# Performance work log

Measured on AMD Instinct MI355X. Metric: run time of the kernel, lower is better.

Reference implementation:

```python
import jax, jax.numpy as jnp
import numpy as np
import math

B, S, D, H = 2, 2048, 2048, 16
DH = D // H
NEG = -1e9  # finite stand-in for -inf so fully-masked rows stay NaN-free


def setup_inputs() -> dict:
    key = jax.random.key(0)
    ks = jax.random.split(key, 6)
    x = jax.random.normal(ks[0], (B, S, D), dtype=jnp.float32)
    key_padding_mask = jax.random.randint(ks[1], (B, S), 0, 2, dtype=jnp.int32)
    Wqkv_w = jax.random.normal(ks[2], (3 * D, D), dtype=jnp.float32) / math.sqrt(D)
    Wqkv_b = jnp.zeros((3 * D,), dtype=jnp.float32)
    out_w = jax.random.normal(ks[3], (D, D), dtype=jnp.float32) / math.sqrt(D)
    out_b = jnp.zeros((D,), dtype=jnp.float32)
    return {"x": x, "key_padding_mask": key_padding_mask, "Wqkv_w": Wqkv_w,
            "Wqkv_b": Wqkv_b, "out_w": out_w, "out_b": out_b}


def reference(x, key_padding_mask, Wqkv_w, Wqkv_b, out_w, out_b):
    b, s, d = x.shape
    # fused QKV projection (torch Linear: y = x @ W.T + b)
    qkv = (x @ Wqkv_w.T + Wqkv_b).reshape(b, s, 3, H, DH)
    q, k, v = qkv[:, :, 0], qkv[:, :, 1], qkv[:, :, 2]  # each [b, s, H, DH]
    scale = 1.0 / math.sqrt(DH)
    scores = jnp.einsum('bqhd,bkhd->bhqk', q, k) * scale  # [b, H, s, s]
    # additive key-padding bias: -inf where mask == 0 (finite NEG for stability)
    pad_bias = jnp.where(key_padding_mask == 0, NEG, 0.0).astype(x.dtype)[:, None, None, :]
    # causal mask: key index > query index is disallowed
    causal = jnp.where(jnp.arange(s)[None, :] > jnp.arange(s)[:, None], NEG, 0.0).astype(x.dtype)
    p = jax.nn.softmax(scores + pad_bias + causal, axis=-1)
    attn = jnp.einsum('bhqk,bkhd->bqhd', p, v).reshape(b, s, d)
    return attn @ out_w.T + out_b
```

## Files before the change

### kernel.cpp

```cpp
#include <hip/hip_runtime.h>
#include <cstdint>

typedef unsigned short u16;
typedef __attribute__((ext_vector_type(8))) short short8v;
typedef __attribute__((ext_vector_type(8))) unsigned short u16x8;
typedef __attribute__((ext_vector_type(4))) float floatx4;

typedef unsigned int __attribute__((address_space(1))) as1_u32;
typedef unsigned int __attribute__((address_space(3))) as3_u32;

__device__ __forceinline__ u16 f2bf(float f) {
  union { float f; unsigned u; } v; v.f = f;
  unsigned r = v.u + 0x7FFFu + ((v.u >> 16) & 1u);
  return (u16)(r >> 16);
}

__device__ __forceinline__ unsigned cvt_pk_bf16(float lo, float hi) {
  unsigned r;
  asm("v_cvt_pk_bf16_f32 %0, %1, %2" : "=v"(r) : "v"(lo), "v"(hi));
  return r;
}

__device__ __forceinline__ void gload16(void* lds, const void* g) {
  __builtin_amdgcn_global_load_lds((as1_u32*)(uintptr_t)g, (as3_u32*)(uintptr_t)lds, 16, 0, 0);
}

__global__ __launch_bounds__(256) void f2bf_kernel(const float* __restrict__ in,
                                                   u16* __restrict__ out, int n4) {
  int i = blockIdx.x * 256 + threadIdx.x;
  const int stride = gridDim.x * 256;
  for (; i < n4; i += stride) {
    float4 v = ((const float4*)in)[i];
    ushort4 o;
    o.x = f2bf(v.x); o.y = f2bf(v.y); o.z = f2bf(v.z); o.w = f2bf(v.w);
    ((ushort4*)out)[i] = o;
  }
}

template <int OUT_BF16>
__global__ __launch_bounds__(256)
void gemm_bt(const u16* __restrict__ A, const u16* __restrict__ B,
             const float* __restrict__ bias, void* __restrict__ C,
             int M, int N, int K) {
  __shared__ u16 As[128 * 32];
  __shared__ u16 Bs[128 * 32];
  const int tid = threadIdx.x;
  const int wave = tid >> 6, lane = tid & 63;
  const int wr = wave >> 1, wc = wave & 1;
  const int li = lane & 15, lg = lane >> 4;
  const int brow = blockIdx.y * 128, bcol = blockIdx.x * 128;

  const int e0 = tid * 8, e1 = 2048 + tid * 8;
  const u16* aSrc0 = A + (size_t)(brow + (e0 >> 5)) * K + (e0 & 31);
  const u16* aSrc1 = A + (size_t)(brow + (e1 >> 5)) * K + (e1 & 31);
  const u16* bSrc0 = B + (size_t)(bcol + (e0 >> 5)) * K + (e0 & 31);
  const u16* bSrc1 = B + (size_t)(bcol + (e1 >> 5)) * K + (e1 & 31);

  floatx4 acc[4][4];
#pragma unroll
  for (int m = 0; m < 4; ++m)
#pragma unroll
    for (int n = 0; n < 4; ++n) acc[m][n] = floatx4{0.f, 0.f, 0.f, 0.f};

  for (int kt = 0; kt < K; kt += 32) {
    gload16((char*)As + tid * 16,        aSrc0 + kt);
    gload16((char*)As + 4096 + tid * 16, aSrc1 + kt);
    gload16((char*)Bs + tid * 16,        bSrc0 + kt);
    gload16((char*)Bs + 4096 + tid * 16, bSrc1 + kt);
    asm volatile("s_waitcnt vmcnt(0)" ::: "memory");
    __syncthreads();

    short8v a[4], b[4];
#pragma unroll
    for (int m = 0; m < 4; ++m)
      a[m] = *(const short8v*)&As[(wr * 64 + m * 16 + li) * 32 + lg * 8];
#pragma unroll
    for (int n = 0; n < 4; ++n)
      b[n] = *(const short8v*)&Bs[(wc * 64 + n * 16 + li) * 32 + lg * 8];
#pragma unroll
    for (int m = 0; m < 4; ++m)
#pragma unroll
      for (int n = 0; n < 4; ++n)
        acc[m][n] = __builtin_amdgcn_mfma_f32_16x16x32_bf16(a[m], b[n], acc[m][n], 0, 0, 0);
    __syncthreads();
  }

  const int crow0 = brow + wr * 64 + lg * 4;
  const int ccol0 = bcol + wc * 64 + li;
#pragma unroll
  for (int n = 0; n < 4; ++n) {
    const float bv = bias[ccol0 + n * 16];
#pragma unroll
    for (int m = 0; m < 4; ++m) {
#pragma unroll
      for (int j = 0; j < 4; ++j) {
        const float v = acc[m][n][j] + bv;
        const size_t idx = (size_t)(crow0 + m * 16 + j) * N + (ccol0 + n * 16);
        if (OUT_BF16) ((u16*)C)[idx] = f2bf(v);
        else          ((float*)C)[idx] = v;
      }
    }
  }
}

__global__ __launch_bounds__(256)
void transpose_v(const u16* __restrict__ qkv, u16* __restrict__ vt) {
  __shared__ u16 T[64][136];
  const int st = blockIdx.x, bh = blockIdx.y;
  const int b = bh >> 4, h = bh & 15;
  const int tid = threadIdx.x;
  const u16* src = qkv + (size_t)(b * 2048 + st * 64) * 6144 + 4096 + h * 128;
  u16* dst = vt + (size_t)bh * 128 * 2048 + st * 64;
#pragma unroll
  for (int p = 0; p < 4; ++p) {
    const int e = (p * 256 + tid) * 8;
    const int r = e >> 7, c = e & 127;
    *(u16x8*)&T[r][c] = *(const u16x8*)&src[(size_t)r * 6144 + c];
  }
  __syncthreads();
#pragma unroll
  for (int p = 0; p < 4; ++p) {
    const int e = (p * 256 + tid) * 8;
    const int dh = e >> 6, s0 = e & 63;
    u16x8 o;
#pragma unroll
    for (int j = 0; j < 8; ++j) o[j] = T[s0 + j][dh];
    *(u16x8*)&dst[(size_t)dh * 2048 + s0] = o;
  }
}

__global__ __launch_bounds__(256, 2)
void attn_fused(const u16* __restrict__ qkv, const u16* __restrict__ vt,
                const int* __restrict__ kpm, u16* __restrict__ attn_out) {
  constexpr int S = 2048, DQ = 6144;
  __shared__ u16 Kl[2][64 * 128];
  __shared__ u16 Vl[128 * 64];
  __shared__ float mskf[2048];
  __shared__ int s_any;
  const int bx = blockIdx.x, by = blockIdx.y;
  const int qt = ((by >> 4) & 1) ? bx : (15 - bx);
  const int bh = by;
  const int b = bh >> 4, h = bh & 15;
  const int tid = threadIdx.x, wave = tid >> 6, lane = tid & 63;
  const int lg = lane >> 4, li = lane & 15;
  const int qrow0 = qt * 128 + wave * 32;

  const u16* Qb = qkv + (size_t)b * S * DQ + h * 128;
  const u16* Kb = Qb + 2048;
  const u16* Vtb = vt + (size_t)bh * 128 * 2048;
  const int* mrow = kpm + b * S;

  if (tid == 0) s_any = 0;
  __syncthreads();
  {
    int a = 0;
    for (int j = tid; j < 2048; j += 256) {
      const int mv = mrow[j];
      mskf[j] = mv ? 0.f : -1.0e9f;
      if (mv && j <= qt * 128) a = 1;
    }
    if (a) s_any = 1;
  }
  __syncthreads();
  const int anyv = s_any;
  const int nt = anyv ? (2 * qt + 2) : 32;
  const int causalFromW = anyv ? (qrow0 >> 6) : 0;

  short8v qb[2][4];
#pragma unroll
  for (int m = 0; m < 2; ++m) {
    const u16* qp = Qb + (size_t)(qrow0 + m * 16 + li) * DQ + lg * 8;
#pragma unroll
    for (int kk = 0; kk < 4; ++kk) qb[m][kk] = *(const short8v*)(qp + kk * 32);
  }
  asm volatile("s_waitcnt vmcnt(0)" ::: "memory");

  float mM[2], lSum[2];
  floatx4 oa[2][8];
#pragma unroll
  for (int m = 0; m < 2; ++m) {
    mM[m] = -3.0e38f; lSum[m] = 0.f;
#pragma unroll
    for (int n = 0; n < 8; ++n) oa[m][n] = floatx4{0.f, 0.f, 0.f, 0.f};
  }

  const u16* kSrc[4]; const u16* vSrc[4];
#pragma unroll
  for (int i = 0; i < 4; ++i) {
    const int L = i * 4096 + tid * 16;
    const int r = L >> 8;
    const int c = ((L & 255) ^ ((r & 7) << 4)) >> 1;
    kSrc[i] = Kb + (size_t)r * DQ + c;
    const int d = L >> 7;
    const int sv = ((L & 127) ^ ((d & 7) << 4)) >> 1;
    vSrc[i] = Vtb + (size_t)d * 2048 + sv;
  }

#define STAGE_K(buf, kt_)                                                      \
  {                                                                            \
    const int kv0_ = (kt_) * 64;                                               \
    _Pragma("unroll")                                                          \
    for (int i = 0; i < 4; ++i)                                                \
      gload16((char*)Kl + (buf) * 16384 + i * 4096 + tid * 16,                 \
              kSrc[i] + (size_t)kv0_ * DQ);                                    \
  }
#define STAGE_V(kt_)                                                           \
  {                                                                            \
    const int kv0_ = (kt_) * 64;                                               \
    _Pragma("unroll")                                                          \
    for (int i = 0; i < 4; ++i)                                                \
      gload16((char*)Vl + i * 4096 + tid * 16, vSrc[i] + kv0_);                \
  }

  const float scale = 0.08838834764831845f;

  STAGE_K(0, 0);
  STAGE_V(0);

  for (int kt = 0; kt < nt; ++kt) {
    const int cur = kt & 1;
    const int kv0 = kt * 64;
    if (kt + 1 < nt) {
      STAGE_K(cur ^ 1, kt + 1);
      asm volatile("s_waitcnt vmcnt(8)" ::: "memory");
    } else {
      asm volatile("s_waitcnt vmcnt(4)" ::: "memory");
    }
    __builtin_amdgcn_s_barrier();

    const char* Kcur = (const char*)Kl + cur * 16384;

    floatx4 sc[2][4];
#pragma unroll
    for (int n = 0; n < 4; ++n) { sc[0][n] = floatx4{0,0,0,0}; sc[1][n] = floatx4{0,0,0,0}; }
#pragma unroll
    for (int n = 0; n < 4; ++n) {
      const int r = n * 16 + li;
#pragma unroll
      for (int kk = 0; kk < 4; ++kk) {
        const int byteo = (r * 256 + kk * 64 + lg * 16) ^ ((r & 7) << 4);
        const short8v kf = *(const short8v*)(Kcur + byteo);
        sc[0][n] = __builtin_amdgcn_mfma_f32_16x16x32_bf16(kf, qb[0][kk], sc[0][n], 0, 0, 0);
        sc[1][n] = __builtin_amdgcn_mfma_f32_16x16x32_bf16(kf, qb[1][kk], sc[1][n], 0, 0, 0);
      }
    }

    floatx4 pbv[4];
#pragma unroll
    for (int n = 0; n < 4; ++n)
      pbv[n] = *(const floatx4*)&mskf[kv0 + n * 16 + lg * 4];
    const bool cz = (kt >= causalFromW);

    short8v pf[2][2];
#pragma unroll
    for (int m = 0; m < 2; ++m) {
      const int q_l = qrow0 + m * 16 + li;
      float tmax = -3.0e38f;
#pragma unroll
      for (int n = 0; n < 4; ++n)
#pragma unroll
        for (int j = 0; j < 4; ++j) {
          float s = sc[m][n][j] * scale + pbv[n][j];
          if (cz && (kv0 + n * 16 + lg * 4 + j > q_l)) s -= 1.0e9f;
          sc[m][n][j] = s;
          tmax = fmaxf(tmax, s);
        }
      tmax = fmaxf(tmax, __shfl_xor(tmax, 16));
      tmax = fmaxf(tmax, __shfl_xor(tmax, 32));
      const float mnew = fmaxf(mM[m], tmax);
      const float f = __expf(mM[m] - mnew);
      mM[m] = mnew;
      float rs = 0.f;
#pragma unroll
      for (int n = 0; n < 4; ++n)
#pragma unroll
        for (int j = 0; j < 4; ++j) {
          const float e = __expf(sc[m][n][j] - mnew);
          sc[m][n][j] = e; rs += e;
        }
      rs += __shfl_xor(rs, 16);
      rs += __shfl_xor(rs, 32);
      lSum[m] = lSum[m] * f + rs;
#pragma unroll
      for (int n2 = 0; n2 < 8; ++n2) oa[m][n2] *= f;

      unsigned w32[4][2];
#pragma unroll
      for (int n = 0; n < 4; ++n) {
        w32[n][0] = cvt_pk_bf16(sc[m][n][0], sc[m][n][1]);
        w32[n][1] = cvt_pk_bf16(sc[m][n][2], sc[m][n][3]);
      }
      union PF { short8v s; unsigned w[4]; } pfu[2];
#pragma unroll
      for (int kk2 = 0; kk2 < 2; ++kk2) {
#pragma unroll
        for (int hh = 0; hh < 2; ++hh) {
          unsigned u = w32[2 * kk2][hh], v = w32[2 * kk2 + 1][hh];
          asm volatile("v_permlane32_swap_b32 %0, %1" : "+v"(u), "+v"(v));
          asm volatile("v_permlane16_swap_b32 %0, %1" : "+v"(u), "+v"(v));
          pfu[kk2].w[hh] = u;
          pfu[kk2].w[2 + hh] = v;
        }
      }
      pf[m][0] = pfu[0].s;
      pf[m][1] = pfu[1].s;
    }

    if (kt + 1 < nt) asm volatile("s_waitcnt vmcnt(4)" ::: "memory");
    else             asm volatile("s_waitcnt vmcnt(0)" ::: "memory");
    __builtin_amdgcn_s_barrier();

#pragma unroll
    for (int kk2 = 0; kk2 < 2; ++kk2) {
#pragma unroll
      for (int n2 = 0; n2 < 8; ++n2) {
        const int d = n2 * 16 + li;
        const int vbyte = (d * 128 + kk2 * 64 + lg * 16) ^ ((d & 7) << 4);
        const short8v vf = *(const short8v*)((const char*)Vl + vbyte);
        oa[0][n2] = __builtin_amdgcn_mfma_f32_16x16x32_bf16(vf, pf[0][kk2], oa[0][n2], 0, 0, 0);
        oa[1][n2] = __builtin_amdgcn_mfma_f32_16x16x32_bf16(vf, pf[1][kk2], oa[1][n2], 0, 0, 0);
      }
    }
    __builtin_amdgcn_s_barrier();
    if (kt + 1 < nt) STAGE_V(kt + 1);
  }

  {
    char* Ol = (char*)Kl + wave * 8192;
#pragma unroll
    for (int m = 0; m < 2; ++m) {
      const float inv = 1.0f / lSum[m];
      const int q_ = m * 16 + li;
#pragma unroll
      for (int n2 = 0; n2 < 8; ++n2) {
        unsigned lo = cvt_pk_bf16(oa[m][n2][0] * inv, oa[m][n2][1] * inv);
        unsigned hi = cvt_pk_bf16(oa[m][n2][2] * inv, oa[m][n2][3] * inv);
        const int byteo = (q_ * 256 + n2 * 32 + lg * 8) ^ ((q_ & 7) << 4);
        uint2 pr; pr.x = lo; pr.y = hi;
        *(uint2*)(Ol + byteo) = pr;
      }
    }
    asm volatile("s_waitcnt lgkmcnt(0)" ::: "memory");
#pragma unroll
    for (int rr = 0; rr < 4; ++rr) {
      const int r = rr * 8 + (lane >> 3);
      const size_t grow = (size_t)(b * 2048 + qt * 128 + wave * 32 + r) * 2048 + h * 128;
#pragma unroll
      for (int s2 = 0; s2 < 2; ++s2) {
        const int byteo = (r * 256 + (lane & 7) * 32 + s2 * 16) ^ ((r & 7) << 4);
        const u16x8 val = *(const u16x8*)(Ol + byteo);
        *(u16x8*)&attn_out[grow + (lane & 7) * 16 + s2 * 8] = val;
      }
    }
  }
#undef STAGE_K
#undef STAGE_V
}

extern "C" void kernel_launch(void* const* d_in, const int* in_sizes, int n_in,
                              void* d_out, int out_size, void* d_ws, size_t ws_size,
                              hipStream_t stream) {
  const float* x    = (const float*)d_in[0];
  const int*   kpm  = (const int*)d_in[1];
  const float* wqkv = (const float*)d_in[2];
  const float* bqkv = (const float*)d_in[3];
  const float* wout = (const float*)d_in[4];
  const float* bout = (const float*)d_in[5];
  float* out = (float*)d_out;

  char* ws = (char*)d_ws;
  u16* xbf   = (u16*)(ws);
  u16* wqbf  = (u16*)(ws + (16u << 20));
  u16* wobf  = (u16*)(ws + (40u << 20));
  u16* qkvb  = (u16*)(ws + (48u << 20));
  u16* vtb   = (u16*)(ws + (96u << 20));
  u16* attnb = (u16*)(ws + (112u << 20));

  f2bf_kernel<<<1024, 256, 0, stream>>>(x,    xbf,  4096 * 2048 / 4);
  f2bf_kernel<<<1024, 256, 0, stream>>>(wqkv, wqbf, 6144 * 2048 / 4);
  f2bf_kernel<<<1024, 256, 0, stream>>>(wout, wobf, 2048 * 2048 / 4);

  gemm_bt<1><<<dim3(48, 32), 256, 0, stream>>>(xbf, wqbf, bqkv, qkvb, 4096, 6144, 2048);
  transpose_v<<<dim3(32, 32), 256, 0, stream>>>(qkvb, vtb);
  attn_fused<<<dim3(16, 32), 256, 0, stream>>>(qkvb, vtb, kpm, attnb);
  gemm_bt<0><<<dim3(16, 32), 256, 0, stream>>>(attnb, wobf, bout, out, 4096, 2048, 2048);
}
```

Measured before the change: 341.7 us.

## Replace GEMM with 256x256-tile, 8-wave, double-buffered swizzled LDS pipeline

Replaces the 128x128 single-buffered GEMM with a 256x256 tile kernel using 512 threads. It uses a 64-wide K step, XOR-swizzled LDS, and double-buffered global-to-LDS loads staggered across four compute phases, with setprio around the MFMA bursts. The aim is to hide global load latency, raise arithmetic intensity and cut bank conflicts. The larger tiles leave only 128 blocks for the output projection, which may underfill the device, and the kernel uses heavy LDS and registers.

```diff
diff --git a/kernel.cpp b/kernel.cpp
--- a/kernel.cpp
+++ b/kernel.cpp
@@ -38,60 +38,120 @@
 }
 
 template <int OUT_BF16>
-__global__ __launch_bounds__(256)
-void gemm_bt(const u16* __restrict__ A, const u16* __restrict__ B,
+__global__ __launch_bounds__(512, 2)
+void gemm256(const u16* __restrict__ A, const u16* __restrict__ B,
              const float* __restrict__ bias, void* __restrict__ C,
              int M, int N, int K) {
-  __shared__ u16 As[128 * 32];
-  __shared__ u16 Bs[128 * 32];
+  __shared__ u16 lds[2][4][8192];
   const int tid = threadIdx.x;
-  const int wave = tid >> 6, lane = tid & 63;
-  const int wr = wave >> 1, wc = wave & 1;
+  const int wid = tid >> 6, lane = tid & 63;
+  const int wr = wid >> 2, wc = wid & 3;
   const int li = lane & 15, lg = lane >> 4;
-  const int brow = blockIdx.y * 128, bcol = blockIdx.x * 128;
-
-  const int e0 = tid * 8, e1 = 2048 + tid * 8;
-  const u16* aSrc0 = A + (size_t)(brow + (e0 >> 5)) * K + (e0 & 31);
-  const u16* aSrc1 = A + (size_t)(brow + (e1 >> 5)) * K + (e1 & 31);
-  const u16* bSrc0 = B + (size_t)(bcol + (e0 >> 5)) * K + (e0 & 31);
-  const u16* bSrc1 = B + (size_t)(bcol + (e1 >> 5)) * K + (e1 & 31);
-
-  floatx4 acc[4][4];
-#pragma unroll
-  for (int m = 0; m < 4; ++m)
+  const int brow = blockIdx.y * 256, bcol = blockIdx.x * 256;
+  const int NT = K >> 6;
+
+  const int rowL = tid >> 3;
+  const int klog = ((((tid & 7) << 4) ^ ((rowL & 7) << 4)) >> 1);
+  const u16* aS = A + (size_t)(brow + rowL) * K + klog;
+  const u16* bS = B + (size_t)(bcol + rowL) * K + klog;
+
+#define STG(slot, reg, src, hh, kt_)                                            \
+  {                                                                             \
+    const u16* s_ = (src) + (size_t)((hh) * 128) * K + (kt_) * 64;              \
+    gload16((char*)&lds[slot][reg][0] + tid * 16, s_);                          \
+    gload16((char*)&lds[slot][reg][0] + 8192 + tid * 16, s_ + (size_t)64 * K);  \
+  }
+
+  floatx4 acc[8][4];
+#pragma unroll
+  for (int m = 0; m < 8; ++m)
 #pragma unroll
     for (int n = 0; n < 4; ++n) acc[m][n] = floatx4{0.f, 0.f, 0.f, 0.f};
 
-  for (int kt = 0; kt < K; kt += 32) {
-    gload16((char*)As + tid * 16,        aSrc0 + kt);
-    gload16((char*)As + 4096 + tid * 16, aSrc1 + kt);
-    gload16((char*)Bs + tid * 16,        bSrc0 + kt);
-    gload16((char*)Bs + 4096 + tid * 16, bSrc1 + kt);
-    asm volatile("s_waitcnt vmcnt(0)" ::: "memory");
-    __syncthreads();
-
-    short8v a[4], b[4];
-#pragma unroll
-    for (int m = 0; m < 4; ++m)
-      a[m] = *(const short8v*)&As[(wr * 64 + m * 16 + li) * 32 + lg * 8];
-#pragma unroll
-    for (int n = 0; n < 4; ++n)
-      b[n] = *(const short8v*)&Bs[(wc * 64 + n * 16 + li) * 32 + lg * 8];
-#pragma unroll
-    for (int m = 0; m < 4; ++m)
-#pragma unroll
-      for (int n = 0; n < 4; ++n)
-        acc[m][n] = __builtin_amdgcn_mfma_f32_16x16x32_bf16(a[m], b[n], acc[m][n], 0, 0, 0);
-    __syncthreads();
-  }
-
-  const int crow0 = brow + wr * 64 + lg * 4;
+  const int kx0 = (lg * 16) ^ ((li & 7) << 4);
+  const int kx1 = (64 + lg * 16) ^ ((li & 7) << 4);
+  const int ar0 = li * 128;
+  const int bc0 = ((wc & 1) * 64 + li) * 128;
+
+  STG(0, 0, aS, 0, 0);
+  STG(0, 1, aS, 1, 0);
+  STG(0, 2, bS, 0, 0);
+  STG(0, 3, bS, 1, 0);
+  STG(1, 2, bS, 0, 1);
+  STG(1, 3, bS, 1, 1);
+  asm volatile("s_waitcnt vmcnt(4)" ::: "memory");
+  __builtin_amdgcn_s_barrier();
+
+  for (int t = 0; t < NT; ++t) {
+    const int cur = t & 1;
+    const char* Ab = (const char*)&lds[cur][wr][0];
+    const char* Bb = (const char*)&lds[cur][2 + (wc >> 1)][0];
+
+    short8v bf[4][2], af[2][2];
+#pragma unroll
+    for (int n = 0; n < 4; ++n) {
+      bf[n][0] = *(const short8v*)(Bb + bc0 + n * 2048 + kx0);
+      bf[n][1] = *(const short8v*)(Bb + bc0 + n * 2048 + kx1);
+    }
+#pragma unroll
+    for (int mm = 0; mm < 2; ++mm) {
+      af[mm][0] = *(const short8v*)(Ab + ar0 + mm * 2048 + kx0);
+      af[mm][1] = *(const short8v*)(Ab + ar0 + mm * 2048 + kx1);
+    }
+    if (t + 1 < NT) STG(cur ^ 1, 0, aS, 0, t + 1);
+    asm volatile("s_waitcnt lgkmcnt(8)" ::: "memory");
+    __builtin_amdgcn_s_barrier();
+    asm volatile("s_waitcnt lgkmcnt(0)" ::: "memory");
+    __builtin_amdgcn_s_setprio(1);
+#pragma unroll
+    for (int mm = 0; mm < 2; ++mm)
+#pragma unroll
+      for (int ks = 0; ks < 2; ++ks)
+#pragma unroll
+        for (int n = 0; n < 4; ++n)
+          acc[mm][n] = __builtin_amdgcn_mfma_f32_16x16x32_bf16(af[mm][ks], bf[n][ks], acc[mm][n], 0, 0, 0);
+    __builtin_amdgcn_s_setprio(0);
+    __builtin_amdgcn_s_barrier();
+
+#pragma unroll
+    for (int ph = 1; ph < 4; ++ph) {
+      const int m0 = ph * 2;
+      short8v a2[2][2];
+#pragma unroll
+      for (int mm = 0; mm < 2; ++mm) {
+        a2[mm][0] = *(const short8v*)(Ab + ar0 + (m0 + mm) * 2048 + kx0);
+        a2[mm][1] = *(const short8v*)(Ab + ar0 + (m0 + mm) * 2048 + kx1);
+      }
+      if (ph == 1)      { if (t + 1 < NT) STG(cur ^ 1, 1, aS, 1, t + 1); }
+      else if (ph == 2) { if (t + 2 < NT) STG(cur, 2, bS, 0, t + 2); }
+      else              { if (t + 2 < NT) STG(cur, 3, bS, 1, t + 2); }
+      __builtin_amdgcn_s_barrier();
+      asm volatile("s_waitcnt lgkmcnt(0)" ::: "memory");
+      __builtin_amdgcn_s_setprio(1);
+#pragma unroll
+      for (int mm = 0; mm < 2; ++mm)
+#pragma unroll
+        for (int ks = 0; ks < 2; ++ks)
+#pragma unroll
+          for (int n = 0; n < 4; ++n)
+            acc[m0 + mm][n] = __builtin_amdgcn_mfma_f32_16x16x32_bf16(a2[mm][ks], bf[n][ks], acc[m0 + mm][n], 0, 0, 0);
+      __builtin_amdgcn_s_setprio(0);
+      if (ph == 3) {
+        if (t + 2 < NT) asm volatile("s_waitcnt vmcnt(4)" ::: "memory");
+        else            asm volatile("s_waitcnt vmcnt(0)" ::: "memory");
+      }
+      __builtin_amdgcn_s_barrier();
+    }
+  }
+#undef STG
+
+  const int crow0 = brow + wr * 128 + lg * 4;
   const int ccol0 = bcol + wc * 64 + li;
 #pragma unroll
   for (int n = 0; n < 4; ++n) {
     const float bv = bias[ccol0 + n * 16];
 #pragma unroll
-    for (int m = 0; m < 4; ++m) {
+    for (int m = 0; m < 8; ++m) {
 #pragma unroll
       for (int j = 0; j < 4; ++j) {
         const float v = acc[m][n][j] + bv;
@@ -380,8 +440,8 @@
   f2bf_kernel<<<1024, 256, 0, stream>>>(wqkv, wqbf, 6144 * 2048 / 4);
   f2bf_kernel<<<1024, 256, 0, stream>>>(wout, wobf, 2048 * 2048 / 4);
 
-  gemm_bt<1><<<dim3(48, 32), 256, 0, stream>>>(xbf, wqbf, bqkv, qkvb, 4096, 6144, 2048);
+  gemm256<1><<<dim3(24, 16), 512, 0, stream>>>(xbf, wqbf, bqkv, qkvb, 4096, 6144, 2048);
   transpose_v<<<dim3(32, 32), 256, 0, stream>>>(qkvb, vtb);
   attn_fused<<<dim3(16, 32), 256, 0, stream>>>(qkvb, vtb, kpm, attnb);
-  gemm_bt<0><<<dim3(16, 32), 256, 0, stream>>>(attnb, wobf, bout, out, 4096, 2048, 2048);
-}
+  gemm256<0><<<dim3(8, 16), 512, 0, stream>>>(attnb, wobf, bout, out, 4096, 2048, 2048);
+}
```

New measurement: 315.5 us. 1.08x faster.

## Replace GEMM with 256x256-tile, triple-buffered, swizzled-LDS 1024-thread kernel

Applied to the files above, without the earlier changes.

Replaces the 128x128 single-buffered GEMM used for both the QKV and output projections with a 256x256-tile kernel run by 16 waves. The kernel keeps three LDS stages, issuing global-to-LDS loads two K-steps ahead so memory latency overlaps the MFMA work, and it drops one of the two barriers per step. It also XOR-swizzles the LDS layout to avoid bank conflicts, remaps block IDs so neighbouring blocks share inputs in L2, and raises wave priority around the MFMA block. In exchange, the output GEMM now launches only 128 large blocks, which can leave many CUs idle, and the 96KB LDS footprint limits occupancy.

```diff
diff --git a/kernel.cpp b/kernel.cpp
--- a/kernel.cpp
+++ b/kernel.cpp
@@ -38,23 +38,36 @@
 }
 
 template <int OUT_BF16>
-__global__ __launch_bounds__(256)
-void gemm_bt(const u16* __restrict__ A, const u16* __restrict__ B,
+__global__ __launch_bounds__(1024, 4)
+void gemm_v3(const u16* __restrict__ A, const u16* __restrict__ B,
              const float* __restrict__ bias, void* __restrict__ C,
              int M, int N, int K) {
-  __shared__ u16 As[128 * 32];
-  __shared__ u16 Bs[128 * 32];
+  __shared__ u16 Al[3][8192];
+  __shared__ u16 Bl[3][8192];
   const int tid = threadIdx.x;
-  const int wave = tid >> 6, lane = tid & 63;
-  const int wr = wave >> 1, wc = wave & 1;
+  const int wid = tid >> 6, lane = tid & 63;
+  const int wr = wid >> 2, wc = wid & 3;
   const int li = lane & 15, lg = lane >> 4;
-  const int brow = blockIdx.y * 128, bcol = blockIdx.x * 128;
-
-  const int e0 = tid * 8, e1 = 2048 + tid * 8;
-  const u16* aSrc0 = A + (size_t)(brow + (e0 >> 5)) * K + (e0 & 31);
-  const u16* aSrc1 = A + (size_t)(brow + (e1 >> 5)) * K + (e1 & 31);
-  const u16* bSrc0 = B + (size_t)(bcol + (e0 >> 5)) * K + (e0 & 31);
-  const u16* bSrc1 = B + (size_t)(bcol + (e1 >> 5)) * K + (e1 & 31);
+  const int nwg = gridDim.x;
+  const int bid = blockIdx.x;
+  const int swz = (bid & 7) * (nwg >> 3) + (bid >> 3);
+  const int mcnt = M >> 8;
+  const int bm = swz % mcnt, bn = swz / mcnt;
+  const int brow = bm * 256, bcol = bn * 256;
+  const int NT = K >> 5;
+
+  const int P = tid * 16;
+  const int pr = P >> 7;
+  const int innerLog = (P & 127) ^ ((pr & 7) << 4);
+  const int srow = (pr << 1) + (innerLog >> 6);
+  const int skb = innerLog & 63;
+  const u16* aS = A + (size_t)(brow + srow) * K + (skb >> 1);
+  const u16* bS = B + (size_t)(bcol + srow) * K + (skb >> 1);
+
+  const int fxor = ((li >> 1) & 7) << 4;
+  const int finner = (((li & 1) << 6) + (lg << 4)) ^ fxor;
+  const int aoff = (wr * 32 + (li >> 1)) * 128 + finner;
+  const int boff = (wc * 32 + (li >> 1)) * 128 + finner;
 
   floatx4 acc[4][4];
 #pragma unroll
@@ -62,27 +75,41 @@
 #pragma unroll
     for (int n = 0; n < 4; ++n) acc[m][n] = floatx4{0.f, 0.f, 0.f, 0.f};
 
-  for (int kt = 0; kt < K; kt += 32) {
-    gload16((char*)As + tid * 16,        aSrc0 + kt);
-    gload16((char*)As + 4096 + tid * 16, aSrc1 + kt);
-    gload16((char*)Bs + tid * 16,        bSrc0 + kt);
-    gload16((char*)Bs + 4096 + tid * 16, bSrc1 + kt);
-    asm volatile("s_waitcnt vmcnt(0)" ::: "memory");
-    __syncthreads();
-
-    short8v a[4], b[4];
+  gload16((char*)&Al[0][0] + P, aS);
+  gload16((char*)&Bl[0][0] + P, bS);
+  gload16((char*)&Al[1][0] + P, aS + 32);
+  gload16((char*)&Bl[1][0] + P, bS + 32);
+  asm volatile("s_waitcnt vmcnt(2)" ::: "memory");
+  __builtin_amdgcn_s_barrier();
+
+  int sl = 0;
+  for (int t = 0; t < NT; ++t) {
+    const char* Ab = (const char*)&Al[sl][0];
+    const char* Bb = (const char*)&Bl[sl][0];
+    short8v af[4], bf[4];
+#pragma unroll
+    for (int m = 0; m < 4; ++m) af[m] = *(const short8v*)(Ab + aoff + m * 1024);
+#pragma unroll
+    for (int n = 0; n < 4; ++n) bf[n] = *(const short8v*)(Bb + boff + n * 1024);
+
+    int s2 = sl + 2; if (s2 >= 3) s2 -= 3;
+    if (t + 2 < NT) {
+      gload16((char*)&Al[s2][0] + P, aS + (t + 2) * 32);
+      gload16((char*)&Bl[s2][0] + P, bS + (t + 2) * 32);
+    }
+
+    __builtin_amdgcn_s_setprio(1);
 #pragma unroll
     for (int m = 0; m < 4; ++m)
-      a[m] = *(const short8v*)&As[(wr * 64 + m * 16 + li) * 32 + lg * 8];
-#pragma unroll
-    for (int n = 0; n < 4; ++n)
-      b[n] = *(const short8v*)&Bs[(wc * 64 + n * 16 + li) * 32 + lg * 8];
-#pragma unroll
-    for (int m = 0; m < 4; ++m)
 #pragma unroll
       for (int n = 0; n < 4; ++n)
-        acc[m][n] = __builtin_amdgcn_mfma_f32_16x16x32_bf16(a[m], b[n], acc[m][n], 0, 0, 0);
-    __syncthreads();
+        acc[m][n] = __builtin_amdgcn_mfma_f32_16x16x32_bf16(af[m], bf[n], acc[m][n], 0, 0, 0);
+    __builtin_amdgcn_s_setprio(0);
+
+    if (t + 2 < NT)      asm volatile("s_waitcnt vmcnt(2)" ::: "memory");
+    else if (t + 1 < NT) asm volatile("s_waitcnt vmcnt(0)" ::: "memory");
+    __builtin_amdgcn_s_barrier();
+    sl = (sl + 1 == 3) ? 0 : sl + 1;
   }
 
   const int crow0 = brow + wr * 64 + lg * 4;
@@ -336,8 +363,8 @@
         unsigned lo = cvt_pk_bf16(oa[m][n2][0] * inv, oa[m][n2][1] * inv);
         unsigned hi = cvt_pk_bf16(oa[m][n2][2] * inv, oa[m][n2][3] * inv);
         const int byteo = (q_ * 256 + n2 * 32 + lg * 8) ^ ((q_ & 7) << 4);
-        uint2 pr; pr.x = lo; pr.y = hi;
-        *(uint2*)(Ol + byteo) = pr;
+        uint2 pr2; pr2.x = lo; pr2.y = hi;
+        *(uint2*)(Ol + byteo) = pr2;
       }
     }
     asm volatile("s_waitcnt lgkmcnt(0)" ::: "memory");
@@ -380,8 +407,8 @@
   f2bf_kernel<<<1024, 256, 0, stream>>>(wqkv, wqbf, 6144 * 2048 / 4);
   f2bf_kernel<<<1024, 256, 0, stream>>>(wout, wobf, 2048 * 2048 / 4);
 
-  gemm_bt<1><<<dim3(48, 32), 256, 0, stream>>>(xbf, wqbf, bqkv, qkvb, 4096, 6144, 2048);
+  gemm_v3<1><<<384, 1024, 0, stream>>>(xbf, wqbf, bqkv, qkvb, 4096, 6144, 2048);
   transpose_v<<<dim3(32, 32), 256, 0, stream>>>(qkvb, vtb);
   attn_fused<<<dim3(16, 32), 256, 0, stream>>>(qkvb, vtb, kpm, attnb);
-  gemm_bt<0><<<dim3(16, 32), 256, 0, stream>>>(attnb, wobf, bout, out, 4096, 2048, 2048);
-}
+  gemm_v3<0><<<128, 1024, 0, stream>>>(attnb, wobf, bout, out, 4096, 2048, 2048);
+}
```

New measurement: 304.4 us. -10.9%, faster.
